# Kernel tuning notes

Measured on AMD Instinct MI355X. Metric: run time of the kernel, lower is better.

Reference implementation:

```python
import jax, jax.numpy as jnp
import numpy as np

B, TX, TY, C, H = 2, 1024, 4096, 768, 12
D = C // H  # head_dim = 64


def setup_inputs() -> dict:
    key = jax.random.key(0)
    ks = jax.random.split(key, 7)
    x = jax.random.normal(ks[0], (B, TX, C), dtype=jnp.float32)
    y = jax.random.normal(ks[1], (B, TY, C), dtype=jnp.float32)
    # sorted float timestamps in [0, TY]
    x_t = jnp.sort(jax.random.uniform(ks[2], (B, TX), dtype=jnp.float32) * TY, axis=-1)
    y_t = jnp.sort(jax.random.uniform(ks[3], (B, TY), dtype=jnp.float32) * TY, axis=-1)
    y_t = y_t.at[:, 0].set(0.0)  # guarantee every query sees >=1 valid key
    Wq = jax.random.normal(ks[4], (C, C), dtype=jnp.float32) * 0.02
    Wkv = jax.random.normal(ks[5], (C, 2 * C), dtype=jnp.float32) * 0.02
    Wproj = jax.random.normal(ks[6], (C, C), dtype=jnp.float32) * 0.02
    # RotaryEmbedding(dim=D, learned_freq=True): init values are the standard inv freqs
    inv_freq = 1.0 / (10000.0 ** (jnp.arange(0, D, 2, dtype=jnp.float32) / D))
    return {"x": x, "x_t": x_t, "y": y, "y_t": y_t, "dist": 512, "min_dist": 0,
            "Wq": Wq, "Wkv": Wkv, "Wproj": Wproj, "inv_freq": inv_freq}


def _rotate_half(t):
    # interleaved pair rotation: (x1, x2) -> (-x2, x1)
    p = t.reshape(t.shape[:-1] + (-1, 2))
    x1, x2 = p[..., 0], p[..., 1]
    return jnp.stack((-x2, x1), axis=-1).reshape(t.shape)


def _apply_rope(t, pos, inv_freq):
    # t: (B,H,T,D), pos: (B,T), inv_freq: (D/2,)
    f = pos[:, None, :, None] * inv_freq          # (B,1,T,D/2)
    f = jnp.repeat(f, 2, axis=-1)                 # (B,1,T,D) interleaved
    return t * jnp.cos(f) + _rotate_half(t) * jnp.sin(f)


def reference(x, x_t, y, y_t, dist, min_dist, Wq, Wkv, Wproj, inv_freq):
    q = (x @ Wq).reshape(B, TX, H, D).transpose(0, 2, 1, 3)   # (B,H,TX,D)
    kv = y @ Wkv
    k = kv[..., :C].reshape(B, TY, H, D).transpose(0, 2, 1, 3)
    v = kv[..., C:].reshape(B, TY, H, D).transpose(0, 2, 1, 3)
    q = _apply_rope(q, x_t, inv_freq)
    k = _apply_rope(k, y_t, inv_freq)
    # time-window mask: valid iff (x_t - min_dist) >= y_t and (x_t - min_dist) <= y_t + dist
    xt = (x_t - min_dist)[:, :, None]             # (B,TX,1)
    yt = y_t[:, None, :]                          # (B,1,TY)
    mask = (xt >= yt) & (xt <= yt + dist)         # (B,TX,TY)
    scores = jnp.einsum('bhqd,bhkd->bhqk', q, k) / jnp.sqrt(jnp.float32(D))
    scores = jnp.where(mask[:, None, :, :], scores, -jnp.inf)
    attn = jax.nn.softmax(scores, axis=-1)
    out = jnp.einsum('bhqk,bhkd->bhqd', attn, v)
    out = out.transpose(0, 2, 1, 3).reshape(B, TX, C)
    return out @ Wproj
```

## Files before the change

kernel.cpp:

```cpp
#include <hip/hip_runtime.h>
#include <hip/hip_bf16.h>
#include <math.h>

#define B_ 2
#define TX_ 1024
#define TY_ 4096
#define C_ 768
#define H_ 12
#define D_ 64
#define NSPLIT 2
#define R_ (B_ * H_ * TX_)

typedef __bf16 bf16x8 __attribute__((ext_vector_type(8)));
typedef float floatx4 __attribute__((ext_vector_type(4)));

__device__ __forceinline__ void async_copy16(const void* g, void* l) {
    __builtin_amdgcn_global_load_lds(
        (const __attribute__((address_space(1))) unsigned int*)g,
        (__attribute__((address_space(3))) unsigned int*)l,
        16, 0, 0);
}

__device__ __forceinline__ bf16x8 cvt8(const float* s) {
    bf16x8 r;
#pragma unroll
    for (int i = 0; i < 8; i++) r[i] = (__bf16)s[i];
    return r;
}

__global__ __launch_bounds__(256)
void prep(const float* __restrict__ x,  __bf16* __restrict__ xb,
          const float* __restrict__ y,  __bf16* __restrict__ yb,
          const float* __restrict__ Wq, __bf16* __restrict__ Wqt,
          const float* __restrict__ Wkv,__bf16* __restrict__ Wkvt,
          const float* __restrict__ Wpr,__bf16* __restrict__ Wprt)
{
    __shared__ float tile[32][33];
    const int bid = blockIdx.x;
    if (bid >= 2304) {
        const int cb = bid - 2304;
        const float* src; __bf16* dst; size_t base;
        if (cb < 768) { src = x; dst = xb; base = (size_t)cb * 2048; }
        else          { src = y; dst = yb; base = (size_t)(cb - 768) * 2048; }
        const size_t i = base + threadIdx.x * 8;
        float4 v0 = *(const float4*)(src + i);
        float4 v1 = *(const float4*)(src + i + 4);
        bf16x8 p;
        p[0] = (__bf16)v0.x; p[1] = (__bf16)v0.y; p[2] = (__bf16)v0.z; p[3] = (__bf16)v0.w;
        p[4] = (__bf16)v1.x; p[5] = (__bf16)v1.y; p[6] = (__bf16)v1.z; p[7] = (__bf16)v1.w;
        *(bf16x8*)(dst + i) = p;
        return;
    }
    const int bxr = bid % 96;
    const int byr = bid / 96;
    const float* W; __bf16* Wt; int N, nb; float scale = 1.0f;
    if (bxr < 24)      { W = Wq;  Wt = Wqt;  N = C_;     nb = bxr;      scale = 0.125f; }
    else if (bxr < 72) { W = Wkv; Wt = Wkvt; N = 2 * C_; nb = bxr - 24; }
    else               { W = Wpr; Wt = Wprt; N = C_;     nb = bxr - 72; }
    const int bx = nb * 32;
    const int by = byr * 32;
    const int tx = threadIdx.x & 31, ty = threadIdx.x >> 5;
#pragma unroll
    for (int i = 0; i < 4; i++)
        tile[ty + i * 8][tx] = W[(size_t)(by + ty + i * 8) * N + bx + tx];
    __syncthreads();
#pragma unroll
    for (int i = 0; i < 4; i++)
        Wt[(size_t)(bx + ty + i * 8) * C_ + by + tx] =
            (__bf16)(tile[tx][ty + i * 8] * scale);
}

__global__ __launch_bounds__(256)
void gemm_qkv(const __bf16* __restrict__ xb, const __bf16* __restrict__ Wqt,
              const __bf16* __restrict__ yb, const __bf16* __restrict__ Wkvt,
              __bf16* __restrict__ Qbh, __bf16* __restrict__ Kbh,
              __bf16* __restrict__ Vtb,
              const float* __restrict__ x_t, const float* __restrict__ y_t,
              const float* __restrict__ inv_freq)
{
    const int bid = (blockIdx.x & 7) * 216 + (blockIdx.x >> 3);
    const bool isQ = (bid < 192);
    const __bf16* A; const __bf16* Bt; const float* t_arr;
    int row0, n0, T, TSH;
    if (isQ) {
        A = xb; Bt = Wqt; t_arr = x_t;
        row0 = (bid / 6) * 64; n0 = (bid % 6) * 128; T = TX_; TSH = 10;
    } else {
        const int r = bid - 192;
        A = yb; Bt = Wkvt; t_arr = y_t;
        row0 = (r / 12) * 64; n0 = (r % 12) * 128; T = TY_; TSH = 12;
    }
    const bool isV = (!isQ) && (n0 >= C_);

    __shared__ __align__(16) float smem_f[9216];
    __bf16* smem_b = (__bf16*)smem_f;

    const int tid  = threadIdx.x;
    const int wave = tid >> 6;
    const int lane = tid & 63;
    const int m16  = lane & 15;
    const int quad = lane >> 4;
    const int wm   = wave >> 1;
    const int wn   = wave & 1;

    floatx4 acc[2][4];
#pragma unroll
    for (int i = 0; i < 2; i++)
#pragma unroll
        for (int j = 0; j < 4; j++) acc[i][j] = (floatx4){0.f, 0.f, 0.f, 0.f};

    const int eA = wave * 512 + lane * 8;
    const int srA = eA >> 5, scA = eA & 31;
    int srB[2], scB[2];
#pragma unroll
    for (int j = 0; j < 2; j++) {
        const int e = j * 2048 + wave * 512 + lane * 8;
        srB[j] = e >> 5; scB[j] = e & 31;
    }

    auto stage = [&](int chunk, int buf) {
        const int kk = chunk * 32;
        async_copy16(A + (size_t)(row0 + srA) * C_ + (kk + scA),
                     (char*)smem_f + buf * 12288 + wave * 1024);
#pragma unroll
        for (int j = 0; j < 2; j++)
            async_copy16(Bt + (size_t)(n0 + srB[j]) * C_ + (kk + scB[j]),
                         (char*)smem_f + buf * 12288 + 4096 + j * 4096 + wave * 1024);
    };

    stage(0, 0);
    stage(1, 1);

    int cur = 0;
    for (int t = 0; t < 24; ++t) {
        if (t < 23) asm volatile("s_waitcnt vmcnt(3)" ::: "memory");
        else        asm volatile("s_waitcnt vmcnt(0)" ::: "memory");
        __builtin_amdgcn_s_barrier();
        asm volatile("" ::: "memory");

        if (t + 2 < 24) {
            int nb = cur + 2; if (nb >= 3) nb -= 3;
            stage(t + 2, nb);
        }

        const __bf16* As = smem_b + cur * 6144;
        const __bf16* Bs = As + 2048;
        bf16x8 af[2], bfr[4];
#pragma unroll
        for (int i = 0; i < 2; i++)
            af[i] = *(const bf16x8*)(As + (size_t)(wm * 32 + i * 16 + m16) * 32 + quad * 8);
#pragma unroll
        for (int j = 0; j < 4; j++)
            bfr[j] = *(const bf16x8*)(Bs + (size_t)(wn * 64 + j * 16 + m16) * 32 + quad * 8);
#pragma unroll
        for (int i = 0; i < 2; i++)
#pragma unroll
            for (int j = 0; j < 4; j++)
                acc[i][j] = __builtin_amdgcn_mfma_f32_16x16x32_bf16(af[i], bfr[j], acc[i][j], 0, 0, 0);

        cur = (cur == 2) ? 0 : cur + 1;
    }

    const int STR = 132;
    float* fs = smem_f;

#pragma unroll
    for (int i = 0; i < 2; i++) {
        __syncthreads();
#pragma unroll
        for (int j = 0; j < 4; j++) {
            const int col_l = wn * 64 + j * 16 + m16;
#pragma unroll
            for (int r = 0; r < 4; r++) {
                const int row_l = quad * 4 + r;
                float v = acc[i][j][r];
                if (!isV) {
                    const float vp = __shfl_xor(v, 1);
                    const int row = row0 + wm * 32 + i * 16 + row_l;
                    const int cc = (n0 + col_l) & (D_ - 1);
                    const float fr = t_arr[row] * inv_freq[cc >> 1];
                    const float sn = __sinf(fr), cs = __cosf(fr);
                    v = (m16 & 1) ? (v * cs + vp * sn) : (v * cs - vp * sn);
                }
                fs[(wm * 16 + row_l) * STR + col_l] = v;
            }
        }
        __syncthreads();

        if (!isV) {
            __bf16* outb = isQ ? Qbh : Kbh;
            const int r32 = tid >> 3;
            const int lane8 = tid & 7;
            const int grow = row0 + (r32 >> 4) * 32 + i * 16 + (r32 & 15);
            const int bb = grow >> TSH;
            const int rk = grow & (T - 1);
            const int h  = (n0 >> 6) + (lane8 >> 2);
            const int d0 = (lane8 & 3) * 16;
            __bf16* gp = outb + ((size_t)(bb * H_ + h) * T + rk) * 64 + d0;
            const float* sp = &fs[r32 * STR + lane8 * 16];
            *(bf16x8*)gp       = cvt8(sp);
            *(bf16x8*)(gp + 8) = cvt8(sp + 8);
        } else {
            const int dcol = tid >> 1;
            const int g16  = tid & 1;
            const int h  = ((n0 - C_) >> 6) + (dcol >> 6);
            const int dd = dcol & 63;
            const int kbase = row0 + g16 * 32 + i * 16;
            const int bb  = kbase >> 12;
            const int kin = kbase & (TY_ - 1);
            float tmp[16];
#pragma unroll
            for (int jj = 0; jj < 16; jj++)
                tmp[jj] = fs[(g16 * 16 + jj) * STR + dcol];
            __bf16* gp = Vtb + ((size_t)(bb * H_ + h) * 64 + dd) * TY_ + kin;
            *(bf16x8*)gp       = cvt8(tmp);
            *(bf16x8*)(gp + 8) = cvt8(tmp + 8);
        }
    }
}

__global__ __launch_bounds__(256)
void attn_mfma(const __bf16* __restrict__ Qb,
               const __bf16* __restrict__ Kb,
               const __bf16* __restrict__ Vt,
               const float* __restrict__ x_t,
               const float* __restrict__ y_t,
               const int* __restrict__ dist_p,
               const int* __restrict__ min_dist_p,
               float* __restrict__ pacc,
               float* __restrict__ pml)
{
    __shared__ __align__(16) __bf16 Kc[32 * 64];
    __shared__ __align__(16) __bf16 Vc[64 * 32];
    __shared__ __align__(16) __bf16 Pt[4][16 * 32];

    const int tid  = threadIdx.x;
    const int wave = tid >> 6;
    const int m16  = tid & 15;
    const int quad = (tid & 63) >> 4;
    const int qt = blockIdx.x, bh = blockIdx.y, split = blockIdx.z;
    const int b = bh / H_;
    const int qblk  = qt * 64;
    const int qbase = qblk + wave * 16;

    const float dist = (float)dist_p[0];
    const float md   = (float)min_dist_p[0];
    const float* yt = y_t + (size_t)b * TY_;
    const float* xt = x_t + (size_t)b * TX_;

    const float xtmin = xt[qblk] - md;
    const float xtmax = xt[qblk + 63] - md;
    int lo = 0, hi = TY_;
    while (lo < hi) { int mid = (lo + hi) >> 1; if (yt[mid] + dist < xtmin) lo = mid + 1; else hi = mid; }
    const int klo = lo;
    lo = 0; hi = TY_;
    while (lo < hi) { int mid = (lo + hi) >> 1; if (yt[mid] <= xtmax) lo = mid + 1; else hi = mid; }
    const int khi = lo - 1;
    const int len = khi - klo + 1;

    int k0 = klo, k1 = klo;
    if (len > 0) {
        const int cnt = (len + NSPLIT - 1) / NSPLIT;
        k0 = klo + split * cnt;
        k1 = min(k0 + cnt, klo + len);
    }

    float xtq[4];
#pragma unroll
    for (int r = 0; r < 4; r++)
        xtq[r] = xt[qbase + quad * 4 + r] - md;

    const __bf16* qp = Qb + ((size_t)bh * TX_ + qbase + m16) * 64;
    const bf16x8 aq0 = *(const bf16x8*)(qp + quad * 8);
    const bf16x8 aq1 = *(const bf16x8*)(qp + 32 + quad * 8);

    float l[4];
    floatx4 o[4];
#pragma unroll
    for (int r = 0; r < 4; r++) l[r] = 0.f;
#pragma unroll
    for (int t = 0; t < 4; t++) o[t] = (floatx4){0.f, 0.f, 0.f, 0.f};

    for (int kc = k0; kc < k1; kc += 32) {
        const float yt0 = yt[min(kc + m16, TY_ - 1)];
        const float yt1 = yt[min(kc + 16 + m16, TY_ - 1)];

        __syncthreads();
        {
            const int krow = tid >> 3;
            const int kg = min(kc + krow, TY_ - 1);
            async_copy16(Kb + ((size_t)bh * TY_ + kg) * 64 + (tid & 7) * 8,
                         (char*)Kc + tid * 16);
            const int d = tid >> 2;
            const int kv = min(kc + (tid & 3) * 8, TY_ - 8);
            async_copy16(Vt + ((size_t)bh * 64 + d) * TY_ + kv,
                         (char*)Vc + tid * 16);
        }
        __syncthreads();

        const bf16x8 bk0h0 = *(const bf16x8*)(Kc + m16 * 64 + quad * 8);
        const bf16x8 bk1h0 = *(const bf16x8*)(Kc + m16 * 64 + 32 + quad * 8);
        const bf16x8 bk0h1 = *(const bf16x8*)(Kc + (16 + m16) * 64 + quad * 8);
        const bf16x8 bk1h1 = *(const bf16x8*)(Kc + (16 + m16) * 64 + 32 + quad * 8);
        floatx4 s0 = (floatx4){0.f, 0.f, 0.f, 0.f};
        floatx4 s1 = (floatx4){0.f, 0.f, 0.f, 0.f};
        s0 = __builtin_amdgcn_mfma_f32_16x16x32_bf16(aq0, bk0h0, s0, 0, 0, 0);
        s0 = __builtin_amdgcn_mfma_f32_16x16x32_bf16(aq1, bk1h0, s0, 0, 0, 0);
        s1 = __builtin_amdgcn_mfma_f32_16x16x32_bf16(aq0, bk0h1, s1, 0, 0, 0);
        s1 = __builtin_amdgcn_mfma_f32_16x16x32_bf16(aq1, bk1h1, s1, 0, 0, 0);

        const int kg0 = kc + m16;
        const int kg1 = kc + 16 + m16;
        __bf16* pt = Pt[wave];
#pragma unroll
        for (int r = 0; r < 4; r++) {
            const bool v0 = (kg0 < k1) && (xtq[r] >= yt0) && (xtq[r] <= yt0 + dist);
            const bool v1 = (kg1 < k1) && (xtq[r] >= yt1) && (xtq[r] <= yt1 + dist);
            const float p0 = v0 ? (float)(__bf16)__expf(s0[r]) : 0.f;
            const float p1 = v1 ? (float)(__bf16)__expf(s1[r]) : 0.f;
            l[r] += p0 + p1;
            pt[(quad * 4 + r) * 32 + m16]      = (__bf16)p0;
            pt[(quad * 4 + r) * 32 + 16 + m16] = (__bf16)p1;
        }
        const bf16x8 ap = *(const bf16x8*)(pt + m16 * 32 + quad * 8);
#pragma unroll
        for (int t = 0; t < 4; t++) {
            const bf16x8 bv = *(const bf16x8*)(Vc + (t * 16 + m16) * 32 + quad * 8);
            o[t] = __builtin_amdgcn_mfma_f32_16x16x32_bf16(ap, bv, o[t], 0, 0, 0);
        }
    }

#pragma unroll
    for (int r = 0; r < 4; r++) {
#pragma unroll
        for (int w = 1; w < 16; w <<= 1)
            l[r] += __shfl_xor(l[r], w);
    }

#pragma unroll
    for (int t = 0; t < 4; t++)
#pragma unroll
        for (int r = 0; r < 4; r++) {
            const size_t gr = (size_t)bh * TX_ + qbase + quad * 4 + r;
            pacc[((size_t)split * R_ + gr) * 64 + t * 16 + m16] = o[t][r];
        }
    if (m16 == 0) {
#pragma unroll
        for (int r = 0; r < 4; r++) {
            const size_t gr = (size_t)bh * TX_ + qbase + quad * 4 + r;
            pml[(size_t)split * R_ + gr] = l[r];
        }
    }
}

__global__ __launch_bounds__(256)
void combine_kernel(const float* __restrict__ pacc,
                    const float* __restrict__ pml,
                    __bf16* __restrict__ O)
{
    const int d   = threadIdx.x;
    const int sub = threadIdx.y;
    const size_t r = (size_t)blockIdx.x * 4 + sub;
    const int bh  = (int)(r / TX_);
    const int txg = (int)(r % TX_);
    const int b = bh / H_, h = bh % H_;

    float L = 0.f, val = 0.f;
#pragma unroll
    for (int s = 0; s < NSPLIT; s++) {
        L   += pml[(size_t)s * R_ + r];
        val += pacc[((size_t)s * R_ + r) * 64 + d];
    }
    const float o = (L > 0.f) ? val / L : 0.f;
    O[(size_t)(b * TX_ + txg) * C_ + h * D_ + d] = (__bf16)o;
}

__global__ __launch_bounds__(256)
void gemm_proj(const __bf16* __restrict__ A,
               const __bf16* __restrict__ Bt,
               float* __restrict__ out0)
{
    __shared__ __align__(16) float smem_f[12288];
    __bf16* smem_b = (__bf16*)smem_f;

    const int tid  = threadIdx.x;
    const int wave = tid >> 6;
    const int lane = tid & 63;
    const int m16  = lane & 15;
    const int quad = lane >> 4;
    const int wm   = wave >> 1;
    const int wn   = wave & 1;
    const int row0 = blockIdx.y * 128;
    const int n0   = blockIdx.x * 128;

    floatx4 acc[4][4];
#pragma unroll
    for (int i = 0; i < 4; i++)
#pragma unroll
        for (int j = 0; j < 4; j++) acc[i][j] = (floatx4){0.f, 0.f, 0.f, 0.f};

    int srow[4], scol[4];
#pragma unroll
    for (int j = 0; j < 4; j++) {
        int e = j * 2048 + wave * 512 + lane * 8;
        int e2 = e & 4095;
        srow[j] = e2 >> 5;
        scol[j] = e2 & 31;
    }

    auto stage = [&](int chunk, int buf) {
        const int kk = chunk * 32;
#pragma unroll
        for (int j = 0; j < 4; j++) {
            const __bf16* src = (j < 2)
                ? A  + (size_t)(row0 + srow[j]) * C_ + (kk + scol[j])
                : Bt + (size_t)(n0   + srow[j]) * C_ + (kk + scol[j]);
            async_copy16(src, (char*)smem_f + buf * 16384 + j * 4096 + wave * 1024);
        }
    };

    stage(0, 0);
    stage(1, 1);

    int cur = 0;
    for (int t = 0; t < 24; ++t) {
        if (t < 23) asm volatile("s_waitcnt vmcnt(4)" ::: "memory");
        else        asm volatile("s_waitcnt vmcnt(0)" ::: "memory");
        __builtin_amdgcn_s_barrier();
        asm volatile("" ::: "memory");

        if (t + 2 < 24) {
            int nb = cur + 2; if (nb >= 3) nb -= 3;
            stage(t + 2, nb);
        }

        const __bf16* As = smem_b + cur * 8192;
        const __bf16* Bs = As + 4096;
        bf16x8 af[4], bfr[4];
#pragma unroll
        for (int i = 0; i < 4; i++)
            af[i] = *(const bf16x8*)(As + (size_t)(wm * 64 + i * 16 + m16) * 32 + quad * 8);
#pragma unroll
        for (int j = 0; j < 4; j++)
            bfr[j] = *(const bf16x8*)(Bs + (size_t)(wn * 64 + j * 16 + m16) * 32 + quad * 8);
#pragma unroll
        for (int i = 0; i < 4; i++)
#pragma unroll
            for (int j = 0; j < 4; j++)
                acc[i][j] = __builtin_amdgcn_mfma_f32_16x16x32_bf16(af[i], bfr[j], acc[i][j], 0, 0, 0);

        cur = (cur == 2) ? 0 : cur + 1;
    }

    const int STR = 132;
    float* fs = smem_f;
#pragma unroll
    for (int i = 0; i < 4; i++) {
        __syncthreads();
#pragma unroll
        for (int j = 0; j < 4; j++) {
            const int col_l = wn * 64 + j * 16 + m16;
#pragma unroll
            for (int r = 0; r < 4; r++)
                fs[(wm * 16 + quad * 4 + r) * STR + col_l] = acc[i][j][r];
        }
        __syncthreads();
        const int r32 = tid >> 3;
        const int lc  = (tid & 7) * 4;
        const int row = row0 + (r32 >> 4) * 64 + i * 16 + (r32 & 15);
        float* gp = out0 + (size_t)row * C_ + n0;
#pragma unroll
        for (int c2 = 0; c2 < 4; c2++) {
            float4 v4 = *(const float4*)&fs[r32 * STR + c2 * 32 + lc];
            *(float4*)(gp + c2 * 32 + lc) = v4;
        }
    }
}

extern "C" void kernel_launch(void* const* d_in, const int* in_sizes, int n_in,
                              void* d_out, int out_size, void* d_ws, size_t ws_size,
                              hipStream_t stream)
{
    const float* x        = (const float*)d_in[0];
    const float* x_t      = (const float*)d_in[1];
    const float* y        = (const float*)d_in[2];
    const float* y_t      = (const float*)d_in[3];
    const int*   dist     = (const int*)d_in[4];
    const int*   min_dist = (const int*)d_in[5];
    const float* Wq       = (const float*)d_in[6];
    const float* Wkv      = (const float*)d_in[7];
    const float* Wproj    = (const float*)d_in[8];
    const float* inv_freq = (const float*)d_in[9];
    float* out = (float*)d_out;

    const size_t QN = (size_t)B_ * TX_ * C_;
    const size_t KN = (size_t)B_ * TY_ * C_;

    float* ws = (float*)d_ws;
    float* pacc = ws; ws += (size_t)NSPLIT * R_ * 64;
    float* pml  = ws; ws += (size_t)NSPLIT * R_;
    __bf16* bws = (__bf16*)ws;
    __bf16* xb    = bws; bws += QN;
    __bf16* yb    = bws; bws += KN;
    __bf16* Wqt   = bws; bws += (size_t)C_ * C_;
    __bf16* Wkvt  = bws; bws += (size_t)C_ * 2 * C_;
    __bf16* Wprt  = bws; bws += (size_t)C_ * C_;
    __bf16* Ob    = bws; bws += QN;
    __bf16* Qbh   = bws; bws += QN;
    __bf16* Kbh   = bws; bws += KN;
    __bf16* Vtb   = bws; bws += KN + 128;

    prep<<<dim3(2304 + 3840), dim3(256), 0, stream>>>(
        x, xb, y, yb, Wq, Wqt, Wkv, Wkvt, Wproj, Wprt);

    gemm_qkv<<<dim3(1728), dim3(256), 0, stream>>>(
        xb, Wqt, yb, Wkvt, Qbh, Kbh, Vtb, x_t, y_t, inv_freq);

    attn_mfma<<<dim3(TX_ / 64, B_ * H_, NSPLIT), dim3(256), 0, stream>>>(
        Qbh, Kbh, Vtb, x_t, y_t, dist, min_dist, pacc, pml);

    combine_kernel<<<dim3((unsigned)(R_ / 4)), dim3(64, 4), 0, stream>>>(
        pacc, pml, Ob);

    gemm_proj<<<dim3(C_ / 128, (B_ * TX_) / 128), dim3(256), 0, stream>>>(
        Ob, Wprt, out);
}
```

Baseline: 186.2 us.

## Triple-buffer attention K/V loads and retile projection GEMM to 64x128 blocks

The attention kernel now stages K, V^T and the key timestamps into a three-deep LDS ring with async global-to-LDS copies and explicit vmcnt waits. This replaces the per-chunk pair of __syncthreads around synchronous staging, so the next chunks load while the current one is computed. The projection GEMM moves to 64x128 tiles with a 4-slot, 3-ahead prefetch and a swizzled 1D grid of 192 blocks, which raises the block count to fill more CUs. The cost is more LDS per block and fragile hand-counted vmcnt values that differ between waves.

Result: faster. 181.7 us (-2.4%).

```diff
diff --git a/kernel.cpp b/kernel.cpp
--- a/kernel.cpp
+++ b/kernel.cpp
@@ -19,6 +19,13 @@
         (const __attribute__((address_space(1))) unsigned int*)g,
         (__attribute__((address_space(3))) unsigned int*)l,
         16, 0, 0);
+}
+
+__device__ __forceinline__ void async_copy4(const void* g, void* l) {
+    __builtin_amdgcn_global_load_lds(
+        (const __attribute__((address_space(1))) unsigned int*)g,
+        (__attribute__((address_space(3))) unsigned int*)l,
+        4, 0, 0);
 }
 
 __device__ __forceinline__ bf16x8 cvt8(const float* s) {
@@ -230,8 +237,9 @@
                float* __restrict__ pacc,
                float* __restrict__ pml)
 {
-    __shared__ __align__(16) __bf16 Kc[32 * 64];
-    __shared__ __align__(16) __bf16 Vc[64 * 32];
+    __shared__ __align__(16) __bf16 Kc3[3 * 32 * 64];
+    __shared__ __align__(16) __bf16 Vc3[3 * 64 * 32];
+    __shared__ __align__(16) float  ytl[3 * 32];
     __shared__ __align__(16) __bf16 Pt[4][16 * 32];
 
     const int tid  = threadIdx.x;
@@ -264,6 +272,7 @@
         k0 = klo + split * cnt;
         k1 = min(k0 + cnt, klo + len);
     }
+    const int nt = (k1 > k0) ? ((k1 - k0 + 31) >> 5) : 0;
 
     float xtq[4];
 #pragma unroll
@@ -279,24 +288,48 @@
 #pragma unroll
     for (int r = 0; r < 4; r++) l[r] = 0.f;
 #pragma unroll
-    for (int t = 0; t < 4; t++) o[t] = (floatx4){0.f, 0.f, 0.f, 0.f};
-
-    for (int kc = k0; kc < k1; kc += 32) {
-        const float yt0 = yt[min(kc + m16, TY_ - 1)];
-        const float yt1 = yt[min(kc + 16 + m16, TY_ - 1)];
-
-        __syncthreads();
-        {
-            const int krow = tid >> 3;
-            const int kg = min(kc + krow, TY_ - 1);
-            async_copy16(Kb + ((size_t)bh * TY_ + kg) * 64 + (tid & 7) * 8,
-                         (char*)Kc + tid * 16);
-            const int d = tid >> 2;
-            const int kv = min(kc + (tid & 3) * 8, TY_ - 8);
-            async_copy16(Vt + ((size_t)bh * 64 + d) * TY_ + kv,
-                         (char*)Vc + tid * 16);
-        }
-        __syncthreads();
+    for (int ot = 0; ot < 4; ot++) o[ot] = (floatx4){0.f, 0.f, 0.f, 0.f};
+
+    auto stageA = [&](int c, int buf) {
+        const int kc = k0 + c * 32;
+        const int krow = tid >> 3;
+        const int kg = min(kc + krow, TY_ - 1);
+        async_copy16(Kb + ((size_t)bh * TY_ + kg) * 64 + (tid & 7) * 8,
+                     (char*)Kc3 + buf * 4096 + tid * 16);
+        const int d = tid >> 2;
+        const int kv = min(kc + (tid & 3) * 8, TY_ - 8);
+        async_copy16(Vt + ((size_t)bh * 64 + d) * TY_ + kv,
+                     (char*)Vc3 + buf * 4096 + tid * 16);
+        if (tid < 32) {
+            const int gk = min(kc + tid, TY_ - 1);
+            async_copy4(yt + gk, (char*)ytl + buf * 128 + tid * 4);
+        }
+    };
+
+    if (nt > 0) stageA(0, 0);
+    if (nt > 1) stageA(1, 1);
+
+    int cur = 0;
+    for (int tc = 0; tc < nt; ++tc) {
+        if (tc < nt - 1) {
+            if (wave == 0) asm volatile("s_waitcnt vmcnt(3)" ::: "memory");
+            else           asm volatile("s_waitcnt vmcnt(2)" ::: "memory");
+        } else {
+            asm volatile("s_waitcnt vmcnt(0)" ::: "memory");
+        }
+        __builtin_amdgcn_s_barrier();
+        asm volatile("" ::: "memory");
+
+        if (tc + 2 < nt) {
+            int nb = cur + 2; if (nb >= 3) nb -= 3;
+            stageA(tc + 2, nb);
+        }
+
+        const int kc = k0 + tc * 32;
+        const __bf16* Kc = Kc3 + cur * 2048;
+        const __bf16* Vc = Vc3 + cur * 2048;
+        const float yt0 = ytl[cur * 32 + m16];
+        const float yt1 = ytl[cur * 32 + 16 + m16];
 
         const bf16x8 bk0h0 = *(const bf16x8*)(Kc + m16 * 64 + quad * 8);
         const bf16x8 bk1h0 = *(const bf16x8*)(Kc + m16 * 64 + 32 + quad * 8);
@@ -324,10 +357,12 @@
         }
         const bf16x8 ap = *(const bf16x8*)(pt + m16 * 32 + quad * 8);
 #pragma unroll
-        for (int t = 0; t < 4; t++) {
-            const bf16x8 bv = *(const bf16x8*)(Vc + (t * 16 + m16) * 32 + quad * 8);
-            o[t] = __builtin_amdgcn_mfma_f32_16x16x32_bf16(ap, bv, o[t], 0, 0, 0);
-        }
+        for (int ot = 0; ot < 4; ot++) {
+            const bf16x8 bv = *(const bf16x8*)(Vc + (ot * 16 + m16) * 32 + quad * 8);
+            o[ot] = __builtin_amdgcn_mfma_f32_16x16x32_bf16(ap, bv, o[ot], 0, 0, 0);
+        }
+
+        cur = (cur == 2) ? 0 : cur + 1;
     }
 
 #pragma unroll
@@ -338,11 +373,11 @@
     }
 
 #pragma unroll
-    for (int t = 0; t < 4; t++)
+    for (int ot = 0; ot < 4; ot++)
 #pragma unroll
         for (int r = 0; r < 4; r++) {
             const size_t gr = (size_t)bh * TX_ + qbase + quad * 4 + r;
-            pacc[((size_t)split * R_ + gr) * 64 + t * 16 + m16] = o[t][r];
+            pacc[((size_t)split * R_ + gr) * 64 + ot * 16 + m16] = o[ot][r];
         }
     if (m16 == 0) {
 #pragma unroll
@@ -380,6 +415,10 @@
                const __bf16* __restrict__ Bt,
                float* __restrict__ out0)
 {
+    const int bid = (blockIdx.x & 7) * 24 + (blockIdx.x >> 3);
+    const int row0 = (bid / 6) * 64;
+    const int n0   = (bid % 6) * 128;
+
     __shared__ __align__(16) float smem_f[12288];
     __bf16* smem_b = (__bf16*)smem_f;
 
@@ -390,72 +429,65 @@
     const int quad = lane >> 4;
     const int wm   = wave >> 1;
     const int wn   = wave & 1;
-    const int row0 = blockIdx.y * 128;
-    const int n0   = blockIdx.x * 128;
-
-    floatx4 acc[4][4];
-#pragma unroll
-    for (int i = 0; i < 4; i++)
+
+    floatx4 acc[2][4];
+#pragma unroll
+    for (int i = 0; i < 2; i++)
 #pragma unroll
         for (int j = 0; j < 4; j++) acc[i][j] = (floatx4){0.f, 0.f, 0.f, 0.f};
 
-    int srow[4], scol[4];
-#pragma unroll
-    for (int j = 0; j < 4; j++) {
-        int e = j * 2048 + wave * 512 + lane * 8;
-        int e2 = e & 4095;
-        srow[j] = e2 >> 5;
-        scol[j] = e2 & 31;
+    const int eA = wave * 512 + lane * 8;
+    const int srA = eA >> 5, scA = eA & 31;
+    int srB[2], scB[2];
+#pragma unroll
+    for (int j = 0; j < 2; j++) {
+        const int e = j * 2048 + wave * 512 + lane * 8;
+        srB[j] = e >> 5; scB[j] = e & 31;
     }
 
     auto stage = [&](int chunk, int buf) {
         const int kk = chunk * 32;
-#pragma unroll
-        for (int j = 0; j < 4; j++) {
-            const __bf16* src = (j < 2)
-                ? A  + (size_t)(row0 + srow[j]) * C_ + (kk + scol[j])
-                : Bt + (size_t)(n0   + srow[j]) * C_ + (kk + scol[j]);
-            async_copy16(src, (char*)smem_f + buf * 16384 + j * 4096 + wave * 1024);
-        }
+        async_copy16(A + (size_t)(row0 + srA) * C_ + (kk + scA),
+                     (char*)smem_f + buf * 12288 + wave * 1024);
+#pragma unroll
+        for (int j = 0; j < 2; j++)
+            async_copy16(Bt + (size_t)(n0 + srB[j]) * C_ + (kk + scB[j]),
+                         (char*)smem_f + buf * 12288 + 4096 + j * 4096 + wave * 1024);
     };
 
     stage(0, 0);
     stage(1, 1);
-
-    int cur = 0;
+    stage(2, 2);
+
     for (int t = 0; t < 24; ++t) {
-        if (t < 23) asm volatile("s_waitcnt vmcnt(4)" ::: "memory");
-        else        asm volatile("s_waitcnt vmcnt(0)" ::: "memory");
+        if (t < 22)      asm volatile("s_waitcnt vmcnt(6)" ::: "memory");
+        else if (t == 22) asm volatile("s_waitcnt vmcnt(3)" ::: "memory");
+        else              asm volatile("s_waitcnt vmcnt(0)" ::: "memory");
         __builtin_amdgcn_s_barrier();
         asm volatile("" ::: "memory");
 
-        if (t + 2 < 24) {
-            int nb = cur + 2; if (nb >= 3) nb -= 3;
-            stage(t + 2, nb);
-        }
-
-        const __bf16* As = smem_b + cur * 8192;
-        const __bf16* Bs = As + 4096;
-        bf16x8 af[4], bfr[4];
-#pragma unroll
-        for (int i = 0; i < 4; i++)
-            af[i] = *(const bf16x8*)(As + (size_t)(wm * 64 + i * 16 + m16) * 32 + quad * 8);
+        if (t + 3 < 24) stage(t + 3, (t + 3) & 3);
+
+        const __bf16* As = smem_b + (t & 3) * 6144;
+        const __bf16* Bs = As + 2048;
+        bf16x8 af[2], bfr[4];
+#pragma unroll
+        for (int i = 0; i < 2; i++)
+            af[i] = *(const bf16x8*)(As + (size_t)(wm * 32 + i * 16 + m16) * 32 + quad * 8);
 #pragma unroll
         for (int j = 0; j < 4; j++)
             bfr[j] = *(const bf16x8*)(Bs + (size_t)(wn * 64 + j * 16 + m16) * 32 + quad * 8);
 #pragma unroll
-        for (int i = 0; i < 4; i++)
+        for (int i = 0; i < 2; i++)
 #pragma unroll
             for (int j = 0; j < 4; j++)
                 acc[i][j] = __builtin_amdgcn_mfma_f32_16x16x32_bf16(af[i], bfr[j], acc[i][j], 0, 0, 0);
-
-        cur = (cur == 2) ? 0 : cur + 1;
     }
 
     const int STR = 132;
     float* fs = smem_f;
 #pragma unroll
-    for (int i = 0; i < 4; i++) {
+    for (int i = 0; i < 2; i++) {
         __syncthreads();
 #pragma unroll
         for (int j = 0; j < 4; j++) {
@@ -467,7 +499,7 @@
         __syncthreads();
         const int r32 = tid >> 3;
         const int lc  = (tid & 7) * 4;
-        const int row = row0 + (r32 >> 4) * 64 + i * 16 + (r32 & 15);
+        const int row = row0 + (r32 >> 4) * 32 + i * 16 + (r32 & 15);
         float* gp = out0 + (size_t)row * C_ + n0;
 #pragma unroll
         for (int c2 = 0; c2 < 4; c2++) {
@@ -522,6 +554,6 @@
     combine_kernel<<<dim3((unsigned)(R_ / 4)), dim3(64, 4), 0, stream>>>(
         pacc, pml, Ob);
 
-    gemm_proj<<<dim3(C_ / 128, (B_ * TX_) / 128), dim3(256), 0, stream>>>(
+    gemm_proj<<<dim3(192), dim3(256), 0, stream>>>(
         Ob, Wprt, out);
 }
```
